# Kernel tuning notes

Hardware: AMD Instinct MI355X
Metric: run time of the kernel (lower is better)

Reference implementation:

```python
import math
import jax
import jax.numpy as jnp
import numpy as np

B, N = 64, 64
R = N * (N - 1)
DIST_THRESH = 0.35


def _pair_indices(n):
    # edge e = i*(n-1) + j - (j > i): row-major over i, ascending j skipping j == i
    ii = np.repeat(np.arange(n), n - 1)
    jm = np.tile(np.arange(n), (n, 1))
    jj = jm[~np.eye(n, dtype=bool)].reshape(-1)
    return ii, jj


def _rot_basis(a):
    # a: [..., 1] angle -> [..., 2, 2] rotation basis rows [cos,sin],[cos(a+pi/2),sin(a+pi/2)]
    first = jnp.concatenate([jnp.cos(a), jnp.sin(a)], axis=-1)
    second = jnp.concatenate([jnp.cos(a + math.pi / 2), jnp.sin(a + math.pi / 2)], axis=-1)
    return jnp.stack([first, second], axis=-2)


def setup_inputs() -> dict:
    ks = jax.random.split(jax.random.key(0), 8)
    nrm = lambda k, shape, s=1.0: (jax.random.normal(k, shape) * s).astype(jnp.float32)
    return dict(
        objects_state=jax.random.uniform(ks[0], (B, N, 8), dtype=jnp.float32),
        objects_shape=nrm(ks[1], (B, N, 10)),
        relation_info=nrm(ks[2], (B, R, 3)),
        s_mean=jnp.zeros((8,), jnp.float32), s_std=jnp.ones((8,), jnp.float32),
        sh_mean=jnp.zeros((10,), jnp.float32), sh_std=jnp.ones((10,), jnp.float32),
        v_mean=jnp.zeros((3,), jnp.float32), v_std=jnp.ones((3,), jnp.float32),
        W1=nrm(ks[3], (32, 256), 32 ** -0.5), b1=jnp.zeros((256,), jnp.float32),
        W2=nrm(ks[4], (256, 128), 256 ** -0.5), b2=jnp.zeros((128,), jnp.float32),
        W3=nrm(ks[5], (141, 256), 141 ** -0.5), b3=jnp.zeros((256,), jnp.float32),
        W4=nrm(ks[6], (256, 3), 256 ** -0.5), b4=jnp.zeros((3,), jnp.float32),
    )


def reference(objects_state, objects_shape, relation_info, s_mean, s_std, sh_mean, sh_std,
              v_mean, v_std, W1, b1, W2, b2, W3, b3, W4, b4):
    n = objects_state.shape[1]
    ii, jj = _pair_indices(n)

    # ---- pre_proces: distance-threshold edge build into dense one-hot matrices ----
    pos = objects_state[:, :, 0:2]
    dist = jnp.sqrt(jnp.sum((pos[:, :, None, :] - pos[:, None, :, :]) ** 2, axis=-1))
    # torch: where(dist<0.35, dist, 0).nonzero() -> keeps dist<0.35 AND dist != 0 (drops self-edges)
    mask = ((dist < DIST_THRESH) & (dist != 0.0)).astype(jnp.float32)
    mask_flat = mask[:, ii, jj]  # [B, R]
    eye = jnp.eye(n, dtype=jnp.float32)
    receiver_relations = mask_flat[:, :, None] * eye[ii][None]  # [B, R, N]
    sender_relations = mask_flat[:, :, None] * eye[jj][None]    # [B, R, N]

    data_state = (objects_state - s_mean) / s_std
    data_shape = (objects_shape - sh_mean) / sh_std

    senders_state = jnp.einsum('brn,bnd->brd', sender_relations, data_state)
    receivers_state = jnp.einsum('brn,bnd->brd', receiver_relations, data_state)
    senders_shape = jnp.einsum('brn,bnd->brd', sender_relations, data_shape)
    receivers_shape = jnp.einsum('brn,bnd->brd', receiver_relations, data_shape)

    basis = _rot_basis(receivers_state[:, :, 2:3])  # [B, R, 2, 2]
    diff_state = senders_state - receivers_state
    temp = jnp.stack([diff_state[:, :, 0:2], diff_state[:, :, 3:5], senders_state[:, :, 6:8]], axis=-1)  # [B,R,2,3]
    tfed = jnp.einsum('brij,brjk->brik', basis, temp)  # [B,R,2,3]
    angle_diff = diff_state[:, :, 2:3]
    diff_feat = jnp.concatenate([
        tfed[:, :, :, 0], tfed[:, :, :, 1], tfed[:, :, :, 2],
        jnp.sin(2 * angle_diff), jnp.cos(2 * angle_diff),
        diff_state[:, :, 5:6],
    ], axis=-1)  # [B, R, 9]
    rel_data = jnp.concatenate([relation_info, diff_feat, receivers_shape, senders_shape], axis=-1)  # [B,R,32]

    obj_basis = _rot_basis(data_state[:, :, 2:3])  # [B, N, 2, 2]
    obj_vel_tfed = jnp.einsum('bnij,bnj->bni', obj_basis, data_state[:, :, 3:5])
    obj_data = jnp.concatenate([obj_vel_tfed, data_state[:, :, 5:6], data_shape], axis=-1)  # [B,N,13]

    # ---- interaction-network Net ----
    effects = jax.nn.relu(rel_data @ W1 + b1) @ W2 + b2  # [B, R, 128]
    agg = jnp.einsum('brn,bre->bne', receiver_relations, effects)  # [B, N, 128]
    out_vel = jax.nn.relu(jnp.concatenate([obj_data, agg], axis=-1) @ W3 + b3) @ W4 + b4  # [B,N,3]

    # ---- post_proces ----
    angles = objects_state[:, 1:, 2:3]
    pred = out_vel[:, 1:, :] * v_std + v_mean  # inv_transform_vel
    basis_back = _rot_basis(-angles)
    vel_back = jnp.einsum('bnij,bnj->bni', basis_back, pred[:, :, :2])
    x_dot = jnp.concatenate([vel_back, pred[:, :, 2:]], axis=-1)  # [B, N-1, 3]

    tp = np.eye(6, dtype=np.float32)
    tp[3:, 3:] = 0.0
    tq = np.zeros((3, 6), dtype=np.float32)
    for i in range(3):
        tq[i, i] = 1.0
        tq[i, 3 + i] = 1.0
    x_next = objects_state[:, 1:, :6] @ jnp.asarray(tp) + x_dot @ jnp.asarray(tq)
    return x_next  # [B, N-1, 6]
```

## Files before the change

kernel.cpp:

```cpp
#include <hip/hip_runtime.h>
#include <math.h>

#define BB 64
#define NN 64
#define NM1 63
#define RR (NN*(NN-1))

typedef short bf16x8 __attribute__((ext_vector_type(8)));
typedef float f32x4 __attribute__((ext_vector_type(4)));

union U4 { uint4 u; bf16x8 b; };

__device__ inline unsigned int f2bf(float f) {
    unsigned int u = __float_as_uint(f);
    return (u + 0x7FFFu + ((u >> 16) & 1u)) >> 16;
}
__device__ inline unsigned int pack2(float a, float b) {
    return f2bf(a) | (f2bf(b) << 16);
}

__global__ __launch_bounds__(256) void gppp_kernel(
    const float* __restrict__ objects_state,
    const float* __restrict__ objects_shape,
    const float* __restrict__ relation_info,
    const float* __restrict__ s_mean, const float* __restrict__ s_std,
    const float* __restrict__ sh_mean, const float* __restrict__ sh_std,
    const float* __restrict__ v_mean, const float* __restrict__ v_std,
    const float* __restrict__ W1, const float* __restrict__ b1,
    const float* __restrict__ W2, const float* __restrict__ b2,
    const float* __restrict__ W3, const float* __restrict__ b3,
    const float* __restrict__ W4, const float* __restrict__ b4,
    float* __restrict__ out)
{
    __shared__ __align__(16) unsigned char smem[52480];
    float* s_posx = (float*)(smem);
    float* s_posy = (float*)(smem+256);
    float* s_rst  = (float*)(smem+512);
    float* s_rsh  = (float*)(smem+640);
    int*   s_cntg = (int*)(smem+832);
    float* s_outv = (float*)(smem+848);
    unsigned int* relb_w = (unsigned int*)(smem+1024);
    const uint4*  relb4  = (const uint4*)(smem+1024);
    float* s_p3   = (float*)(smem+1024);
    unsigned int* w1b_w = (unsigned int*)(smem+21504);
    const uint4*  w1b4  = (const uint4*)(smem+21504);
    float* s_p2   = (float*)(smem+21504);
    float* s_h    = (float*)(smem+29696);
    float* s_base = (float*)(smem+41984);
    float* s_hsum = (float*)(smem+46080);
    const float4* s_hsum4 = (const float4*)(smem+46080);
    float* s_nsh  = (float*)(smem+46080);
    float* s_q    = (float*)(smem+50176);
    const float4* s_q4 = (const float4*)(smem+50176);
    float* s_nst  = (float*)(smem+50176);

    const int b  = blockIdx.x >> 4;
    const int bq = blockIdx.x & 15;
    const int nb = bq * 4;
    const int t  = threadIdx.x;
    const int wv = t >> 6, lane = t & 63;
    const int col16 = lane & 15, quad = lane >> 4;

    if (t < 64) {
        s_posx[t] = objects_state[(size_t)(b*NN+t)*8 + 0];
        s_posy[t] = objects_state[(size_t)(b*NN+t)*8 + 1];
    }
    if (t >= 64 && t < 96) {
        int g = (t-64) >> 3, c = t & 7;
        s_rst[g*8+c] = (objects_state[(size_t)(b*NN+nb+g)*8 + c] - s_mean[c]) / s_std[c];
    }
    if (t >= 96 && t < 136) {
        int idx = t - 96; int g = idx/10, c = idx - g*10;
        s_rsh[g*12+c] = (objects_shape[(size_t)(b*NN+nb+g)*10 + c] - sh_mean[c]) / sh_std[c];
    }
    if (t >= 136 && t < 140) s_cntg[t-136] = 0;
    #pragma unroll
    for (int i2 = 0; i2 < 2; ++i2) {
        int idx = t + i2*256;
        int o = idx >> 3, c = idx & 7;
        s_nst[o*9+c] = (objects_state[(size_t)(b*NN+o)*8 + c] - s_mean[c]) / s_std[c];
    }
    #pragma unroll
    for (int i2 = 0; i2 < 3; ++i2) {
        int idx = t + i2*256;
        if (idx < 640) {
            int o = idx/10, c = idx - o*10;
            s_nsh[o*11+c] = (objects_shape[(size_t)(b*NN+o)*10 + c] - sh_mean[c]) / sh_std[c];
        }
    }
    {
        float v[22];
        #pragma unroll
        for (int kc = 0; kc < 22; ++kc) {
            int orig = kc < 12 ? kc : kc + 10;
            v[kc] = W1[orig*256 + t];
        }
        #pragma unroll
        for (int w = 0; w < 11; ++w) w1b_w[t*20 + w] = pack2(v[2*w], v[2*w+1]);
        #pragma unroll
        for (int w = 11; w < 16; ++w) w1b_w[t*20 + w] = 0;
    }
    __syncthreads();

    {
        float wvv[10];
        #pragma unroll
        for (int c = 0; c < 10; ++c) wvv[c] = W1[(12+c)*256 + t];
        const float bb = b1[t];
        #pragma unroll
        for (int g = 0; g < 4; ++g) {
            float acc = bb;
            #pragma unroll
            for (int c = 0; c < 10; ++c) acc = fmaf(s_rsh[g*12+c], wvv[c], acc);
            s_base[g*256+t] = acc;
        }
    }
    if (t < 252) {
        const int g = t/63, k = t - g*63;
        const int n = nb + g;
        const int j = k + (k >= n);
        const float dx = s_posx[n] - s_posx[j];
        const float dy = s_posy[n] - s_posy[j];
        const float dist = sqrtf(dx*dx + dy*dy);
        if (dist < 0.35f && dist != 0.0f) {
            const int slot = atomicAdd(&s_cntg[g], 1);
            const int row = g*64 + slot;
            float f[22];
            const size_t rb = ((size_t)b*RR + n*NM1 + k)*3;
            f[0] = relation_info[rb];
            f[1] = relation_info[rb+1];
            f[2] = relation_info[rb+2];
            float sd[8];
            #pragma unroll
            for (int c = 0; c < 8; ++c) sd[c] = s_nst[j*9+c];
            const float rd0 = s_rst[g*8+0], rd1 = s_rst[g*8+1], rd2 = s_rst[g*8+2],
                        rd3 = s_rst[g*8+3], rd4 = s_rst[g*8+4], rd5 = s_rst[g*8+5];
            const float d0 = sd[0]-rd0, d1 = sd[1]-rd1, d2 = sd[2]-rd2,
                        d3 = sd[3]-rd3, d4 = sd[4]-rd4, d5 = sd[5]-rd5;
            const float ca = cosf(rd2), sa = sinf(rd2);
            f[3]  =  ca*d0 + sa*d1;
            f[4]  = -sa*d0 + ca*d1;
            f[5]  =  ca*d3 + sa*d4;
            f[6]  = -sa*d3 + ca*d4;
            f[7]  =  ca*sd[6] + sa*sd[7];
            f[8]  = -sa*sd[6] + ca*sd[7];
            f[9]  = sinf(2.f*d2);
            f[10] = cosf(2.f*d2);
            f[11] = d5;
            #pragma unroll
            for (int c = 0; c < 10; ++c) f[12+c] = s_nsh[j*11+c];
            #pragma unroll
            for (int w = 0; w < 11; ++w) relb_w[row*20+w] = pack2(f[2*w], f[2*w+1]);
            #pragma unroll
            for (int w = 11; w < 16; ++w) relb_w[row*20+w] = 0;
        }
    }
    __syncthreads();

    {
        int cg[4];
        #pragma unroll
        for (int g = 0; g < 4; ++g) cg[g] = s_cntg[g];
        #pragma unroll
        for (int q4 = 0; q4 < 4; ++q4) {
            const int nt  = wv*4 + q4;
            const int col = nt*16 + col16;
            U4 bu; bu.u = w1b4[col*5 + quad];
            float hb[4], hs[4];
            #pragma unroll
            for (int g = 0; g < 4; ++g) { hb[g] = s_base[g*256+col]; hs[g] = 0.f; }
            #pragma unroll
            for (int g = 0; g < 4; ++g) {
                const int mts = (cg[g] + 15) >> 4;
                for (int mt = 0; mt < mts; ++mt) {
                    const int row = g*64 + mt*16 + col16;
                    U4 au; au.u = relb4[row*5 + quad];
                    f32x4 acc = {0.f, 0.f, 0.f, 0.f};
                    acc = __builtin_amdgcn_mfma_f32_16x16x32_bf16(au.b, bu.b, acc, 0, 0, 0);
                    const int rb2 = mt*16 + quad*4;
                    #pragma unroll
                    for (int i2 = 0; i2 < 4; ++i2) {
                        const float vv = fmaxf(acc[i2] + hb[g], 0.f);
                        hs[g] += (rb2 + i2 < cg[g]) ? vv : 0.f;
                    }
                }
            }
            #pragma unroll
            for (int g = 0; g < 4; ++g) {
                float vv = hs[g];
                vv += __shfl_xor(vv, 16);
                vv += __shfl_xor(vv, 32);
                if (quad == 0) s_hsum[g*256 + col] = vv;
            }
        }
    }
    __syncthreads();

    {
        const int k0 = wv * 64;
        float a0[4], a1[4];
        #pragma unroll
        for (int g = 0; g < 4; ++g) { a0[g] = 0.f; a1[g] = 0.f; }
        for (int k4 = 0; k4 < 16; ++k4) {
            float hv[4][4];
            #pragma unroll
            for (int g = 0; g < 4; ++g) {
                const float4 x = s_hsum4[g*64 + (k0 >> 2) + k4];
                hv[g][0] = x.x; hv[g][1] = x.y; hv[g][2] = x.z; hv[g][3] = x.w;
            }
            #pragma unroll
            for (int i2 = 0; i2 < 4; ++i2) {
                const int k = k0 + k4*4 + i2;
                const float wa = W2[(size_t)k*128 + lane];
                const float wb = W2[(size_t)k*128 + 64 + lane];
                #pragma unroll
                for (int g = 0; g < 4; ++g) {
                    a0[g] = fmaf(hv[g][i2], wa, a0[g]);
                    a1[g] = fmaf(hv[g][i2], wb, a1[g]);
                }
            }
        }
        #pragma unroll
        for (int g = 0; g < 4; ++g) {
            s_p2[(wv*4+g)*128 + lane]      = a0[g];
            s_p2[(wv*4+g)*128 + 64 + lane] = a1[g];
        }
    }
    if (t < 52) {
        const int g = t/13, c = t - g*13;
        const float rd2 = s_rst[g*8+2], rd3 = s_rst[g*8+3],
                    rd4 = s_rst[g*8+4], rd5 = s_rst[g*8+5];
        float v;
        if (c < 2) {
            const float ca = cosf(rd2), sa = sinf(rd2);
            v = (c == 0) ? (ca*rd3 + sa*rd4) : (-sa*rd3 + ca*rd4);
        } else if (c == 2) v = rd5;
        else v = s_rsh[g*12 + (c-3)];
        s_q[g*144 + c] = v;
    }
    __syncthreads();

    #pragma unroll
    for (int i2 = 0; i2 < 2; ++i2) {
        const int o = t + i2*256;
        const int g = o >> 7, e = o & 127;
        float acc = (float)s_cntg[g] * b2[e];
        #pragma unroll
        for (int w = 0; w < 4; ++w) acc += s_p2[(w*4+g)*128 + e];
        s_q[g*144 + 13 + e] = acc;
    }
    __syncthreads();

    {
        const int kstart = wv * 36;
        const int nch = (wv == 3) ? 8 : 9;
        float acc[4][4];
        #pragma unroll
        for (int g = 0; g < 4; ++g)
            #pragma unroll
            for (int cr = 0; cr < 4; ++cr) acc[g][cr] = 0.f;
        for (int cch = 0; cch < nch; ++cch) {
            float qv[4][4];
            #pragma unroll
            for (int g = 0; g < 4; ++g) {
                const float4 x = s_q4[g*36 + (kstart >> 2) + cch];
                qv[g][0] = x.x; qv[g][1] = x.y; qv[g][2] = x.z; qv[g][3] = x.w;
            }
            #pragma unroll
            for (int i2 = 0; i2 < 4; ++i2) {
                const int k = kstart + cch*4 + i2;
                float w3v[4];
                #pragma unroll
                for (int cr = 0; cr < 4; ++cr) w3v[cr] = W3[(size_t)k*256 + lane + cr*64];
                #pragma unroll
                for (int g = 0; g < 4; ++g)
                    #pragma unroll
                    for (int cr = 0; cr < 4; ++cr)
                        acc[g][cr] = fmaf(qv[g][i2], w3v[cr], acc[g][cr]);
            }
        }
        if (wv == 3) {
            float w3v[4];
            #pragma unroll
            for (int cr = 0; cr < 4; ++cr) w3v[cr] = W3[(size_t)140*256 + lane + cr*64];
            #pragma unroll
            for (int g = 0; g < 4; ++g) {
                const float qs = s_q[g*144 + 140];
                #pragma unroll
                for (int cr = 0; cr < 4; ++cr) acc[g][cr] = fmaf(qs, w3v[cr], acc[g][cr]);
            }
        }
        #pragma unroll
        for (int g = 0; g < 4; ++g)
            #pragma unroll
            for (int cr = 0; cr < 4; ++cr)
                s_p3[(wv*4+g)*256 + lane + cr*64] = acc[g][cr];
    }
    __syncthreads();

    {
        const float b3v = b3[t];
        #pragma unroll
        for (int g = 0; g < 4; ++g) {
            float acc = b3v;
            #pragma unroll
            for (int w = 0; w < 4; ++w) acc += s_p3[(w*4+g)*256 + t];
            s_h[g*256 + t] = fmaxf(acc, 0.f);
        }
    }
    __syncthreads();

    {
        float p0 = 0.f, p1 = 0.f, p2 = 0.f;
        #pragma unroll
        for (int cr = 0; cr < 4; ++cr) {
            const int col = lane + cr*64;
            const float h = s_h[wv*256 + col];
            p0 = fmaf(h, W4[col*3+0], p0);
            p1 = fmaf(h, W4[col*3+1], p1);
            p2 = fmaf(h, W4[col*3+2], p2);
        }
        #pragma unroll
        for (int off = 32; off > 0; off >>= 1) {
            p0 += __shfl_down(p0, off);
            p1 += __shfl_down(p1, off);
            p2 += __shfl_down(p2, off);
        }
        if (lane == 0) {
            s_outv[wv*4+0] = p0 + b4[0];
            s_outv[wv*4+1] = p1 + b4[1];
            s_outv[wv*4+2] = p2 + b4[2];
        }
    }
    __syncthreads();

    if (t < 24) {
        const int g = t/6, i = t - g*6;
        const int n = nb + g;
        if (n >= 1) {
            const float q0 = s_outv[g*4+0]*v_std[0] + v_mean[0];
            const float q1 = s_outv[g*4+1]*v_std[1] + v_mean[1];
            const float q2 = s_outv[g*4+2]*v_std[2] + v_mean[2];
            const float ang = objects_state[(size_t)(b*NN+n)*8 + 2];
            const float ca = cosf(ang), sa = sinf(ang);
            const float xd0 = ca*q0 - sa*q1;
            const float xd1 = sa*q0 + ca*q1;
            const int im = i % 3;
            const float xd = (im == 0) ? xd0 : (im == 1) ? xd1 : q2;
            const float base = (i < 3) ? objects_state[(size_t)(b*NN+n)*8 + i] : 0.f;
            out[((size_t)b*NM1 + (n-1))*6 + i] = base + xd;
        }
    }
}

extern "C" void kernel_launch(void* const* d_in, const int* in_sizes, int n_in,
                              void* d_out, int out_size, void* d_ws, size_t ws_size,
                              hipStream_t stream) {
    gppp_kernel<<<dim3(BB*16), dim3(256), 0, stream>>>(
        (const float*)d_in[0],  (const float*)d_in[1],  (const float*)d_in[2],
        (const float*)d_in[3],  (const float*)d_in[4],  (const float*)d_in[5],
        (const float*)d_in[6],  (const float*)d_in[7],  (const float*)d_in[8],
        (const float*)d_in[9],  (const float*)d_in[10], (const float*)d_in[11],
        (const float*)d_in[12], (const float*)d_in[13], (const float*)d_in[14],
        (const float*)d_in[15], (const float*)d_in[16],
        (float*)d_out);
}
```

Baseline: 120.2 us.

## Split into pack, relation and object kernels using bf16 MFMA for W2/W3

A small pre-kernel now packs W1, W2 and W3 into bf16 MFMA fragment layout in the workspace. The relation kernel folds the receiver-shape term into the W1 MFMA by widening K to 32, then writes the per-object effect sums to global memory. A separate object kernel runs the W2 and W3 layers as bf16 MFMA over 16 objects per block, with the W4 projection fused in. This replaces the scalar fp32 W2/W3 loops and the per-block W1 repacking, at the cost of two extra launches, a global round trip for the sums, and bf16 rounding in the later layers.

```diff
diff --git a/kernel.cpp b/kernel.cpp
--- a/kernel.cpp
+++ b/kernel.cpp
@@ -6,9 +6,14 @@
 #define NM1 63
 #define RR (NN*(NN-1))
 
+#define WS1_OFF 0
+#define WS2_OFF 16384
+#define WS3_OFF 81920
+#define WSH_OFF 163840
+#define WSC_OFF 2260992
+
 typedef short bf16x8 __attribute__((ext_vector_type(8)));
 typedef float f32x4 __attribute__((ext_vector_type(4)));
-
 union U4 { uint4 u; bf16x8 b; };
 
 __device__ inline unsigned int f2bf(float f) {
@@ -19,47 +24,68 @@
     return f2bf(a) | (f2bf(b) << 16);
 }
 
-__global__ __launch_bounds__(256) void gppp_kernel(
+__global__ __launch_bounds__(64) void pack_kernel(
+    const float* __restrict__ W1, const float* __restrict__ W2,
+    const float* __restrict__ W3, unsigned char* __restrict__ ws)
+{
+    const int u = blockIdx.x, l = threadIdx.x;
+    const int col16 = l & 15, quad = l >> 4;
+    float v[8];
+    uint4* dst;
+    if (u < 16) {
+        const int nt = u, col = nt*16 + col16;
+        #pragma unroll
+        for (int j = 0; j < 8; ++j) {
+            const int k = quad*8 + j;
+            const int orig = k < 12 ? k : (k < 22 ? k+10 : k-10);
+            v[j] = W1[orig*256 + col];
+        }
+        dst = (uint4*)(ws + WS1_OFF) + (nt*64 + l);
+    } else if (u < 80) {
+        const int w = u-16, nt = w >> 3, kc = w & 7, col = nt*16 + col16;
+        #pragma unroll
+        for (int j = 0; j < 8; ++j) {
+            const int k = kc*32 + quad*8 + j;
+            v[j] = W2[(size_t)k*128 + col];
+        }
+        dst = (uint4*)(ws + WS2_OFF) + ((nt*8 + kc)*64 + l);
+    } else {
+        const int w = u-80, nt = w/5, kc = w - nt*5, col = nt*16 + col16;
+        #pragma unroll
+        for (int j = 0; j < 8; ++j) {
+            const int k = kc*32 + quad*8 + j;
+            v[j] = (k < 141) ? W3[(size_t)k*256 + col] : 0.f;
+        }
+        dst = (uint4*)(ws + WS3_OFF) + ((nt*5 + kc)*64 + l);
+    }
+    uint4 o;
+    o.x = pack2(v[0], v[1]); o.y = pack2(v[2], v[3]);
+    o.z = pack2(v[4], v[5]); o.w = pack2(v[6], v[7]);
+    *dst = o;
+}
+
+__global__ __launch_bounds__(256) void rel_kernel(
     const float* __restrict__ objects_state,
     const float* __restrict__ objects_shape,
     const float* __restrict__ relation_info,
     const float* __restrict__ s_mean, const float* __restrict__ s_std,
     const float* __restrict__ sh_mean, const float* __restrict__ sh_std,
-    const float* __restrict__ v_mean, const float* __restrict__ v_std,
-    const float* __restrict__ W1, const float* __restrict__ b1,
-    const float* __restrict__ W2, const float* __restrict__ b2,
-    const float* __restrict__ W3, const float* __restrict__ b3,
-    const float* __restrict__ W4, const float* __restrict__ b4,
-    float* __restrict__ out)
+    const float* __restrict__ b1,
+    unsigned char* __restrict__ ws)
 {
-    __shared__ __align__(16) unsigned char smem[52480];
-    float* s_posx = (float*)(smem);
-    float* s_posy = (float*)(smem+256);
-    float* s_rst  = (float*)(smem+512);
-    float* s_rsh  = (float*)(smem+640);
-    int*   s_cntg = (int*)(smem+832);
-    float* s_outv = (float*)(smem+848);
-    unsigned int* relb_w = (unsigned int*)(smem+1024);
-    const uint4*  relb4  = (const uint4*)(smem+1024);
-    float* s_p3   = (float*)(smem+1024);
-    unsigned int* w1b_w = (unsigned int*)(smem+21504);
-    const uint4*  w1b4  = (const uint4*)(smem+21504);
-    float* s_p2   = (float*)(smem+21504);
-    float* s_h    = (float*)(smem+29696);
-    float* s_base = (float*)(smem+41984);
-    float* s_hsum = (float*)(smem+46080);
-    const float4* s_hsum4 = (const float4*)(smem+46080);
-    float* s_nsh  = (float*)(smem+46080);
-    float* s_q    = (float*)(smem+50176);
-    const float4* s_q4 = (const float4*)(smem+50176);
-    float* s_nst  = (float*)(smem+50176);
+    __shared__ float s_posx[64], s_posy[64];
+    __shared__ float s_rst[4][8];
+    __shared__ float s_rsh[4][12];
+    __shared__ int   s_cntg[4];
+    __shared__ float s_nst[64][9];
+    __shared__ float s_nsh[64][11];
+    __shared__ __align__(16) unsigned int relb_w[256*20];
+    __shared__ float s_hsum[4][256];
 
     const int b  = blockIdx.x >> 4;
-    const int bq = blockIdx.x & 15;
-    const int nb = bq * 4;
+    const int nb = (blockIdx.x & 15) * 4;
     const int t  = threadIdx.x;
-    const int wv = t >> 6, lane = t & 63;
-    const int col16 = lane & 15, quad = lane >> 4;
+    const int wv = t >> 6, lane = t & 63, col16 = lane & 15, quad = lane >> 4;
 
     if (t < 64) {
         s_posx[t] = objects_state[(size_t)(b*NN+t)*8 + 0];
@@ -67,74 +93,46 @@
     }
     if (t >= 64 && t < 96) {
         int g = (t-64) >> 3, c = t & 7;
-        s_rst[g*8+c] = (objects_state[(size_t)(b*NN+nb+g)*8 + c] - s_mean[c]) / s_std[c];
+        s_rst[g][c] = (objects_state[(size_t)(b*NN+nb+g)*8 + c] - s_mean[c]) / s_std[c];
     }
     if (t >= 96 && t < 136) {
-        int idx = t - 96; int g = idx/10, c = idx - g*10;
-        s_rsh[g*12+c] = (objects_shape[(size_t)(b*NN+nb+g)*10 + c] - sh_mean[c]) / sh_std[c];
+        int idx = t-96, g = idx/10, c = idx - g*10;
+        s_rsh[g][c] = (objects_shape[(size_t)(b*NN+nb+g)*10 + c] - sh_mean[c]) / sh_std[c];
     }
     if (t >= 136 && t < 140) s_cntg[t-136] = 0;
     #pragma unroll
-    for (int i2 = 0; i2 < 2; ++i2) {
-        int idx = t + i2*256;
-        int o = idx >> 3, c = idx & 7;
-        s_nst[o*9+c] = (objects_state[(size_t)(b*NN+o)*8 + c] - s_mean[c]) / s_std[c];
+    for (int r = 0; r < 2; ++r) {
+        int idx = t + r*256, o = idx >> 3, c = idx & 7;
+        s_nst[o][c] = (objects_state[(size_t)(b*NN+o)*8 + c] - s_mean[c]) / s_std[c];
     }
     #pragma unroll
-    for (int i2 = 0; i2 < 3; ++i2) {
-        int idx = t + i2*256;
+    for (int r = 0; r < 3; ++r) {
+        int idx = t + r*256;
         if (idx < 640) {
             int o = idx/10, c = idx - o*10;
-            s_nsh[o*11+c] = (objects_shape[(size_t)(b*NN+o)*10 + c] - sh_mean[c]) / sh_std[c];
-        }
-    }
-    {
-        float v[22];
-        #pragma unroll
-        for (int kc = 0; kc < 22; ++kc) {
-            int orig = kc < 12 ? kc : kc + 10;
-            v[kc] = W1[orig*256 + t];
-        }
-        #pragma unroll
-        for (int w = 0; w < 11; ++w) w1b_w[t*20 + w] = pack2(v[2*w], v[2*w+1]);
-        #pragma unroll
-        for (int w = 11; w < 16; ++w) w1b_w[t*20 + w] = 0;
-    }
-    __syncthreads();
-
-    {
-        float wvv[10];
-        #pragma unroll
-        for (int c = 0; c < 10; ++c) wvv[c] = W1[(12+c)*256 + t];
-        const float bb = b1[t];
-        #pragma unroll
-        for (int g = 0; g < 4; ++g) {
-            float acc = bb;
-            #pragma unroll
-            for (int c = 0; c < 10; ++c) acc = fmaf(s_rsh[g*12+c], wvv[c], acc);
-            s_base[g*256+t] = acc;
-        }
-    }
+            s_nsh[o][c] = (objects_shape[(size_t)(b*NN+o)*10 + c] - sh_mean[c]) / sh_std[c];
+        }
+    }
+    __syncthreads();
+
     if (t < 252) {
-        const int g = t/63, k = t - g*63;
-        const int n = nb + g;
-        const int j = k + (k >= n);
+        const int g = t/63, k = t - g*63, n = nb + g, j = k + (k >= n);
         const float dx = s_posx[n] - s_posx[j];
         const float dy = s_posy[n] - s_posy[j];
         const float dist = sqrtf(dx*dx + dy*dy);
         if (dist < 0.35f && dist != 0.0f) {
             const int slot = atomicAdd(&s_cntg[g], 1);
             const int row = g*64 + slot;
-            float f[22];
+            float f[32];
             const size_t rb = ((size_t)b*RR + n*NM1 + k)*3;
             f[0] = relation_info[rb];
             f[1] = relation_info[rb+1];
             f[2] = relation_info[rb+2];
             float sd[8];
             #pragma unroll
-            for (int c = 0; c < 8; ++c) sd[c] = s_nst[j*9+c];
-            const float rd0 = s_rst[g*8+0], rd1 = s_rst[g*8+1], rd2 = s_rst[g*8+2],
-                        rd3 = s_rst[g*8+3], rd4 = s_rst[g*8+4], rd5 = s_rst[g*8+5];
+            for (int c = 0; c < 8; ++c) sd[c] = s_nst[j][c];
+            const float rd0 = s_rst[g][0], rd1 = s_rst[g][1], rd2 = s_rst[g][2],
+                        rd3 = s_rst[g][3], rd4 = s_rst[g][4], rd5 = s_rst[g][5];
             const float d0 = sd[0]-rd0, d1 = sd[1]-rd1, d2 = sd[2]-rd2,
                         d3 = sd[3]-rd3, d4 = sd[4]-rd4, d5 = sd[5]-rd5;
             const float ca = cosf(rd2), sa = sinf(rd2);
@@ -148,11 +146,19 @@
             f[10] = cosf(2.f*d2);
             f[11] = d5;
             #pragma unroll
-            for (int c = 0; c < 10; ++c) f[12+c] = s_nsh[j*11+c];
-            #pragma unroll
-            for (int w = 0; w < 11; ++w) relb_w[row*20+w] = pack2(f[2*w], f[2*w+1]);
-            #pragma unroll
-            for (int w = 11; w < 16; ++w) relb_w[row*20+w] = 0;
+            for (int c = 0; c < 10; ++c) f[12+c] = s_nsh[j][c];
+            #pragma unroll
+            for (int c = 0; c < 10; ++c) f[22+c] = s_rsh[g][c];
+            uint4* dst = (uint4*)&relb_w[row*20];
+            #pragma unroll
+            for (int w4 = 0; w4 < 4; ++w4) {
+                uint4 o;
+                o.x = pack2(f[w4*8+0], f[w4*8+1]);
+                o.y = pack2(f[w4*8+2], f[w4*8+3]);
+                o.z = pack2(f[w4*8+4], f[w4*8+5]);
+                o.w = pack2(f[w4*8+6], f[w4*8+7]);
+                dst[w4] = o;
+            }
         }
     }
     __syncthreads();
@@ -161,27 +167,25 @@
         int cg[4];
         #pragma unroll
         for (int g = 0; g < 4; ++g) cg[g] = s_cntg[g];
+        const uint4* w1f = (const uint4*)(ws + WS1_OFF);
         #pragma unroll
         for (int q4 = 0; q4 < 4; ++q4) {
-            const int nt  = wv*4 + q4;
-            const int col = nt*16 + col16;
-            U4 bu; bu.u = w1b4[col*5 + quad];
-            float hb[4], hs[4];
-            #pragma unroll
-            for (int g = 0; g < 4; ++g) { hb[g] = s_base[g*256+col]; hs[g] = 0.f; }
+            const int nt = wv*4 + q4, col = nt*16 + col16;
+            U4 bu; bu.u = w1f[nt*64 + lane];
+            const float b1v = b1[col];
+            float hs[4] = {0.f, 0.f, 0.f, 0.f};
             #pragma unroll
             for (int g = 0; g < 4; ++g) {
                 const int mts = (cg[g] + 15) >> 4;
                 for (int mt = 0; mt < mts; ++mt) {
-                    const int row = g*64 + mt*16 + col16;
-                    U4 au; au.u = relb4[row*5 + quad];
+                    U4 au; au.u = *(const uint4*)&relb_w[(g*64 + mt*16 + col16)*20 + quad*4];
                     f32x4 acc = {0.f, 0.f, 0.f, 0.f};
                     acc = __builtin_amdgcn_mfma_f32_16x16x32_bf16(au.b, bu.b, acc, 0, 0, 0);
                     const int rb2 = mt*16 + quad*4;
                     #pragma unroll
-                    for (int i2 = 0; i2 < 4; ++i2) {
-                        const float vv = fmaxf(acc[i2] + hb[g], 0.f);
-                        hs[g] += (rb2 + i2 < cg[g]) ? vv : 0.f;
+                    for (int i = 0; i < 4; ++i) {
+                        const float vv = fmaxf(acc[i] + b1v, 0.f);
+                        hs[g] += (rb2 + i < cg[g]) ? vv : 0.f;
                     }
                 }
             }
@@ -190,165 +194,166 @@
                 float vv = hs[g];
                 vv += __shfl_xor(vv, 16);
                 vv += __shfl_xor(vv, 32);
-                if (quad == 0) s_hsum[g*256 + col] = vv;
+                if (quad == 0) s_hsum[g][col] = vv;
             }
         }
     }
     __syncthreads();
 
     {
-        const int k0 = wv * 64;
-        float a0[4], a1[4];
-        #pragma unroll
-        for (int g = 0; g < 4; ++g) { a0[g] = 0.f; a1[g] = 0.f; }
-        for (int k4 = 0; k4 < 16; ++k4) {
-            float hv[4][4];
-            #pragma unroll
-            for (int g = 0; g < 4; ++g) {
-                const float4 x = s_hsum4[g*64 + (k0 >> 2) + k4];
-                hv[g][0] = x.x; hv[g][1] = x.y; hv[g][2] = x.z; hv[g][3] = x.w;
-            }
-            #pragma unroll
-            for (int i2 = 0; i2 < 4; ++i2) {
-                const int k = k0 + k4*4 + i2;
-                const float wa = W2[(size_t)k*128 + lane];
-                const float wb = W2[(size_t)k*128 + 64 + lane];
-                #pragma unroll
-                for (int g = 0; g < 4; ++g) {
-                    a0[g] = fmaf(hv[g][i2], wa, a0[g]);
-                    a1[g] = fmaf(hv[g][i2], wb, a1[g]);
-                }
-            }
-        }
-        #pragma unroll
-        for (int g = 0; g < 4; ++g) {
-            s_p2[(wv*4+g)*128 + lane]      = a0[g];
-            s_p2[(wv*4+g)*128 + 64 + lane] = a1[g];
-        }
-    }
-    if (t < 52) {
-        const int g = t/13, c = t - g*13;
-        const float rd2 = s_rst[g*8+2], rd3 = s_rst[g*8+3],
-                    rd4 = s_rst[g*8+4], rd5 = s_rst[g*8+5];
-        float v;
-        if (c < 2) {
-            const float ca = cosf(rd2), sa = sinf(rd2);
-            v = (c == 0) ? (ca*rd3 + sa*rd4) : (-sa*rd3 + ca*rd4);
-        } else if (c == 2) v = rd5;
-        else v = s_rsh[g*12 + (c-3)];
-        s_q[g*144 + c] = v;
-    }
-    __syncthreads();
+        unsigned int* hdst = (unsigned int*)(ws + WSH_OFF);
+        #pragma unroll
+        for (int r = 0; r < 2; ++r) {
+            const int idx = r*256 + t, g = idx >> 7, i = idx & 127;
+            const int obj = b*NN + nb + g;
+            hdst[obj*128 + i] = pack2(s_hsum[g][2*i], s_hsum[g][2*i+1]);
+        }
+        if (t < 4) ((int*)(ws + WSC_OFF))[b*NN + nb + t] = s_cntg[t];
+    }
+}
+
+__global__ __launch_bounds__(256) void obj_kernel(
+    const float* __restrict__ objects_state,
+    const float* __restrict__ objects_shape,
+    const float* __restrict__ s_mean, const float* __restrict__ s_std,
+    const float* __restrict__ sh_mean, const float* __restrict__ sh_std,
+    const float* __restrict__ v_mean, const float* __restrict__ v_std,
+    const float* __restrict__ b2, const float* __restrict__ b3,
+    const float* __restrict__ W4, const float* __restrict__ b4,
+    const unsigned char* __restrict__ ws,
+    float* __restrict__ out)
+{
+    __shared__ __align__(16) unsigned short s_q[16*168];
+    __shared__ float s_red[4][16][3];
+    __shared__ float s_outv[16][3];
+
+    const int bi = blockIdx.x >> 2, ot = blockIdx.x & 3;
+    const int obj0 = bi*NN + ot*16;
+    const int t = threadIdx.x, wv = t >> 6, lane = t & 63,
+              col16 = lane & 15, quad = lane >> 4;
 
     #pragma unroll
-    for (int i2 = 0; i2 < 2; ++i2) {
-        const int o = t + i2*256;
-        const int g = o >> 7, e = o & 127;
-        float acc = (float)s_cntg[g] * b2[e];
-        #pragma unroll
-        for (int w = 0; w < 4; ++w) acc += s_p2[(w*4+g)*128 + e];
-        s_q[g*144 + 13 + e] = acc;
-    }
-    __syncthreads();
+    for (int r = 0; r < 2; ++r) {
+        const int idx = r*256 + t;
+        if (idx < 432) {
+            const int m = idx/27, c = 141 + (idx - m*27);
+            s_q[m*168 + c] = 0;
+        }
+    }
+
+    if (t >= 64 && t < 80) {
+        const int o = t - 64, n = ot*16 + o;
+        const size_t sb = (size_t)(bi*NN + n)*8;
+        const float rd2 = (objects_state[sb+2] - s_mean[2]) / s_std[2];
+        const float rd3 = (objects_state[sb+3] - s_mean[3]) / s_std[3];
+        const float rd4 = (objects_state[sb+4] - s_mean[4]) / s_std[4];
+        const float rd5 = (objects_state[sb+5] - s_mean[5]) / s_std[5];
+        const float ca = cosf(rd2), sa = sinf(rd2);
+        s_q[o*168 + 0] = (unsigned short)f2bf( ca*rd3 + sa*rd4);
+        s_q[o*168 + 1] = (unsigned short)f2bf(-sa*rd3 + ca*rd4);
+        s_q[o*168 + 2] = (unsigned short)f2bf(rd5);
+        #pragma unroll
+        for (int c = 0; c < 10; ++c)
+            s_q[o*168 + 3 + c] = (unsigned short)f2bf(
+                (objects_shape[(size_t)(bi*NN+n)*10 + c] - sh_mean[c]) / sh_std[c]);
+    }
 
     {
-        const int kstart = wv * 36;
-        const int nch = (wv == 3) ? 8 : 9;
-        float acc[4][4];
-        #pragma unroll
-        for (int g = 0; g < 4; ++g)
-            #pragma unroll
-            for (int cr = 0; cr < 4; ++cr) acc[g][cr] = 0.f;
-        for (int cch = 0; cch < nch; ++cch) {
-            float qv[4][4];
-            #pragma unroll
-            for (int g = 0; g < 4; ++g) {
-                const float4 x = s_q4[g*36 + (kstart >> 2) + cch];
-                qv[g][0] = x.x; qv[g][1] = x.y; qv[g][2] = x.z; qv[g][3] = x.w;
-            }
-            #pragma unroll
-            for (int i2 = 0; i2 < 4; ++i2) {
-                const int k = kstart + cch*4 + i2;
-                float w3v[4];
-                #pragma unroll
-                for (int cr = 0; cr < 4; ++cr) w3v[cr] = W3[(size_t)k*256 + lane + cr*64];
-                #pragma unroll
-                for (int g = 0; g < 4; ++g)
-                    #pragma unroll
-                    for (int cr = 0; cr < 4; ++cr)
-                        acc[g][cr] = fmaf(qv[g][i2], w3v[cr], acc[g][cr]);
-            }
-        }
-        if (wv == 3) {
-            float w3v[4];
-            #pragma unroll
-            for (int cr = 0; cr < 4; ++cr) w3v[cr] = W3[(size_t)140*256 + lane + cr*64];
-            #pragma unroll
-            for (int g = 0; g < 4; ++g) {
-                const float qs = s_q[g*144 + 140];
-                #pragma unroll
-                for (int cr = 0; cr < 4; ++cr) acc[g][cr] = fmaf(qs, w3v[cr], acc[g][cr]);
-            }
-        }
-        #pragma unroll
-        for (int g = 0; g < 4; ++g)
-            #pragma unroll
-            for (int cr = 0; cr < 4; ++cr)
-                s_p3[(wv*4+g)*256 + lane + cr*64] = acc[g][cr];
+        const uint4* hsrc = (const uint4*)(ws + WSH_OFF);
+        U4 af[8];
+        #pragma unroll
+        for (int kc = 0; kc < 8; ++kc)
+            af[kc].u = hsrc[(size_t)(obj0 + col16)*32 + kc*4 + quad];
+        float cntv[4];
+        #pragma unroll
+        for (int i = 0; i < 4; ++i)
+            cntv[i] = (float)((const int*)(ws + WSC_OFF))[obj0 + quad*4 + i];
+        const uint4* w2f = (const uint4*)(ws + WS2_OFF);
+        #pragma unroll
+        for (int ntl = 0; ntl < 2; ++ntl) {
+            const int nt = wv*2 + ntl, col = nt*16 + col16;
+            f32x4 acc = {0.f, 0.f, 0.f, 0.f};
+            #pragma unroll
+            for (int kc = 0; kc < 8; ++kc) {
+                U4 bu; bu.u = w2f[(nt*8 + kc)*64 + lane];
+                acc = __builtin_amdgcn_mfma_f32_16x16x32_bf16(af[kc].b, bu.b, acc, 0, 0, 0);
+            }
+            const float b2v = b2[col];
+            #pragma unroll
+            for (int i = 0; i < 4; ++i) {
+                const int row = quad*4 + i;
+                s_q[row*168 + 13 + col] = (unsigned short)f2bf(acc[i] + cntv[i]*b2v);
+            }
+        }
     }
     __syncthreads();
 
     {
-        const float b3v = b3[t];
-        #pragma unroll
-        for (int g = 0; g < 4; ++g) {
-            float acc = b3v;
-            #pragma unroll
-            for (int w = 0; w < 4; ++w) acc += s_p3[(w*4+g)*256 + t];
-            s_h[g*256 + t] = fmaxf(acc, 0.f);
-        }
-    }
-    __syncthreads();
-
-    {
-        float p0 = 0.f, p1 = 0.f, p2 = 0.f;
-        #pragma unroll
-        for (int cr = 0; cr < 4; ++cr) {
-            const int col = lane + cr*64;
-            const float h = s_h[wv*256 + col];
-            p0 = fmaf(h, W4[col*3+0], p0);
-            p1 = fmaf(h, W4[col*3+1], p1);
-            p2 = fmaf(h, W4[col*3+2], p2);
-        }
-        #pragma unroll
-        for (int off = 32; off > 0; off >>= 1) {
-            p0 += __shfl_down(p0, off);
-            p1 += __shfl_down(p1, off);
-            p2 += __shfl_down(p2, off);
-        }
-        if (lane == 0) {
-            s_outv[wv*4+0] = p0 + b4[0];
-            s_outv[wv*4+1] = p1 + b4[1];
-            s_outv[wv*4+2] = p2 + b4[2];
-        }
-    }
-    __syncthreads();
-
-    if (t < 24) {
-        const int g = t/6, i = t - g*6;
-        const int n = nb + g;
+        U4 af3[5];
+        #pragma unroll
+        for (int kc = 0; kc < 5; ++kc)
+            af3[kc].u = *(const uint4*)&s_q[col16*168 + kc*32 + quad*8];
+        const uint4* w3f = (const uint4*)(ws + WS3_OFF);
+        float p[4][3];
+        #pragma unroll
+        for (int i = 0; i < 4; ++i) { p[i][0]=0.f; p[i][1]=0.f; p[i][2]=0.f; }
+        #pragma unroll
+        for (int ntl = 0; ntl < 4; ++ntl) {
+            const int nt = wv*4 + ntl, col = nt*16 + col16;
+            f32x4 acc = {0.f, 0.f, 0.f, 0.f};
+            #pragma unroll
+            for (int kc = 0; kc < 5; ++kc) {
+                U4 bu; bu.u = w3f[(nt*5 + kc)*64 + lane];
+                acc = __builtin_amdgcn_mfma_f32_16x16x32_bf16(af3[kc].b, bu.b, acc, 0, 0, 0);
+            }
+            const float b3v = b3[col];
+            const float w40 = W4[col*3+0], w41 = W4[col*3+1], w42 = W4[col*3+2];
+            #pragma unroll
+            for (int i = 0; i < 4; ++i) {
+                const float h = fmaxf(acc[i] + b3v, 0.f);
+                p[i][0] = fmaf(h, w40, p[i][0]);
+                p[i][1] = fmaf(h, w41, p[i][1]);
+                p[i][2] = fmaf(h, w42, p[i][2]);
+            }
+        }
+        #pragma unroll
+        for (int off = 1; off < 16; off <<= 1)
+            #pragma unroll
+            for (int i = 0; i < 4; ++i) {
+                p[i][0] += __shfl_xor(p[i][0], off);
+                p[i][1] += __shfl_xor(p[i][1], off);
+                p[i][2] += __shfl_xor(p[i][2], off);
+            }
+        if (col16 == 0)
+            #pragma unroll
+            for (int i = 0; i < 4; ++i) {
+                s_red[wv][quad*4+i][0] = p[i][0];
+                s_red[wv][quad*4+i][1] = p[i][1];
+                s_red[wv][quad*4+i][2] = p[i][2];
+            }
+    }
+    __syncthreads();
+    if (t < 48) {
+        const int m = t/3, o = t - m*3;
+        s_outv[m][o] = b4[o] + s_red[0][m][o] + s_red[1][m][o]
+                             + s_red[2][m][o] + s_red[3][m][o];
+    }
+    __syncthreads();
+
+    if (t < 96) {
+        const int m = t/6, i = t - m*6, n = ot*16 + m;
         if (n >= 1) {
-            const float q0 = s_outv[g*4+0]*v_std[0] + v_mean[0];
-            const float q1 = s_outv[g*4+1]*v_std[1] + v_mean[1];
-            const float q2 = s_outv[g*4+2]*v_std[2] + v_mean[2];
-            const float ang = objects_state[(size_t)(b*NN+n)*8 + 2];
+            const float q0 = s_outv[m][0]*v_std[0] + v_mean[0];
+            const float q1 = s_outv[m][1]*v_std[1] + v_mean[1];
+            const float q2 = s_outv[m][2]*v_std[2] + v_mean[2];
+            const float ang = objects_state[(size_t)(bi*NN+n)*8 + 2];
             const float ca = cosf(ang), sa = sinf(ang);
             const float xd0 = ca*q0 - sa*q1;
             const float xd1 = sa*q0 + ca*q1;
             const int im = i % 3;
             const float xd = (im == 0) ? xd0 : (im == 1) ? xd1 : q2;
-            const float base = (i < 3) ? objects_state[(size_t)(b*NN+n)*8 + i] : 0.f;
-            out[((size_t)b*NM1 + (n-1))*6 + i] = base + xd;
+            const float base = (i < 3) ? objects_state[(size_t)(bi*NN+n)*8 + i] : 0.f;
+            out[((size_t)bi*NM1 + (n-1))*6 + i] = base + xd;
         }
     }
 }
@@ -356,12 +361,31 @@
 extern "C" void kernel_launch(void* const* d_in, const int* in_sizes, int n_in,
                               void* d_out, int out_size, void* d_ws, size_t ws_size,
                               hipStream_t stream) {
-    gppp_kernel<<<dim3(BB*16), dim3(256), 0, stream>>>(
-        (const float*)d_in[0],  (const float*)d_in[1],  (const float*)d_in[2],
-        (const float*)d_in[3],  (const float*)d_in[4],  (const float*)d_in[5],
-        (const float*)d_in[6],  (const float*)d_in[7],  (const float*)d_in[8],
-        (const float*)d_in[9],  (const float*)d_in[10], (const float*)d_in[11],
-        (const float*)d_in[12], (const float*)d_in[13], (const float*)d_in[14],
-        (const float*)d_in[15], (const float*)d_in[16],
-        (float*)d_out);
-}
+    const float* objects_state = (const float*)d_in[0];
+    const float* objects_shape = (const float*)d_in[1];
+    const float* relation_info = (const float*)d_in[2];
+    const float* s_mean  = (const float*)d_in[3];
+    const float* s_std   = (const float*)d_in[4];
+    const float* sh_mean = (const float*)d_in[5];
+    const float* sh_std  = (const float*)d_in[6];
+    const float* v_mean  = (const float*)d_in[7];
+    const float* v_std   = (const float*)d_in[8];
+    const float* W1 = (const float*)d_in[9];
+    const float* b1 = (const float*)d_in[10];
+    const float* W2 = (const float*)d_in[11];
+    const float* b2 = (const float*)d_in[12];
+    const float* W3 = (const float*)d_in[13];
+    const float* b3 = (const float*)d_in[14];
+    const float* W4 = (const float*)d_in[15];
+    const float* b4 = (const float*)d_in[16];
+    unsigned char* ws = (unsigned char*)d_ws;
+
+    pack_kernel<<<dim3(160), dim3(64), 0, stream>>>(W1, W2, W3, ws);
+    rel_kernel<<<dim3(BB*16), dim3(256), 0, stream>>>(
+        objects_state, objects_shape, relation_info,
+        s_mean, s_std, sh_mean, sh_std, b1, ws);
+    obj_kernel<<<dim3(BB*4), dim3(256), 0, stream>>>(
+        objects_state, objects_shape,
+        s_mean, s_std, sh_mean, sh_std, v_mean, v_std,
+        b2, b3, W4, b4, ws, (float*)d_out);
+}
```

New measurement: 109.6 us. 8.8% less time.
